# Kernel tuning notes

Measured on AMD Instinct MI355X. Metric: run time of the kernel, lower is better.

The kernel has to match this reference:

```python
import jax, jax.numpy as jnp
import numpy as np
import math

D_MODEL = 2048
N_HEADS = 16
D_K = D_MODEL // N_HEADS
B = 4
S = 2048


def setup_inputs() -> dict:
    key = jax.random.key(0)
    ks = jax.random.split(key, 12)
    sd = 1.0 / math.sqrt(D_MODEL)
    inp = {
        "query": jax.random.normal(ks[0], (B, S, D_MODEL), dtype=jnp.float32),
        "key": jax.random.normal(ks[1], (B, S, D_MODEL), dtype=jnp.float32),
        "value": jax.random.normal(ks[2], (B, S, D_MODEL), dtype=jnp.float32),
        # causal mask: 1 where attendable, 0 where masked (mask == 0 -> -1e9)
        "mask": jnp.tril(jnp.ones((1, 1, S, S), dtype=jnp.int32)),
        "W_q": jax.random.uniform(ks[3], (D_MODEL, D_MODEL), jnp.float32, -sd, sd),
        "b_q": jnp.zeros((D_MODEL,), jnp.float32),
        "W_k": jax.random.uniform(ks[4], (D_MODEL, D_MODEL), jnp.float32, -sd, sd),
        "b_k": jnp.zeros((D_MODEL,), jnp.float32),
        "W_v": jax.random.uniform(ks[5], (D_MODEL, D_MODEL), jnp.float32, -sd, sd),
        "b_v": jnp.zeros((D_MODEL,), jnp.float32),
        "W_o": jax.random.uniform(ks[6], (D_MODEL, D_MODEL), jnp.float32, -sd, sd),
        "b_o": jnp.zeros((D_MODEL,), jnp.float32),
    }
    return inp


def reference(query, key, value, mask, W_q, b_q, W_k, b_k, W_v, b_v, W_o, b_o):
    scale = math.sqrt(D_K)
    # QKV projections + split heads: [B, S, D] -> [B, H, S, d_k]
    def split_heads(x):
        return x.reshape(B, -1, N_HEADS, D_K).transpose(0, 2, 1, 3)

    Q = split_heads(query @ W_q.T + b_q)
    K = split_heads(key @ W_k.T + b_k)
    V = split_heads(value @ W_v.T + b_v)

    # scores: [B, H, Sq, Sk]
    scores = jnp.einsum("bhqd,bhkd->bhqk", Q, K) / scale
    scores = jnp.where(mask == 0, jnp.float32(-1e9), scores)
    attn = jax.nn.softmax(scores, axis=-1)
    # context: [B, H, Sq, d_k] -> [B, Sq, D]
    ctx = jnp.einsum("bhqk,bhkd->bhqd", attn, V)
    ctx = ctx.transpose(0, 2, 1, 3).reshape(B, S, D_MODEL)
    return ctx @ W_o.T + b_o
```

## Files before the change

### kernel.cpp

```cpp
#include <hip/hip_runtime.h>
#include <stdint.h>

#define D_MODEL 2048
#define S_LEN 2048
#define BATCH 4
#define NHEADS 16
#define DK 128
#define M_TOK (BATCH * S_LEN)

typedef __attribute__((ext_vector_type(8))) short bf16x8;
typedef __attribute__((ext_vector_type(4))) float f32x4;

__device__ __forceinline__ short f2bf(float f) {
  unsigned u = __float_as_uint(f);
  u = (u + 0x7FFF + ((u >> 16) & 1)) >> 16;
  return (short)u;
}

__device__ __forceinline__ void gl2lds16(const void* g, void* l) {
  __builtin_amdgcn_global_load_lds(
      (const __attribute__((address_space(1))) unsigned int*)g,
      (__attribute__((address_space(3))) unsigned int*)l, 16, 0, 0);
}

#define ASM_BAR() asm volatile("s_barrier" ::: "memory")
#define VMCNT2() asm volatile("s_waitcnt vmcnt(2)" ::: "memory")
#define VMCNT0() asm volatile("s_waitcnt vmcnt(0)" ::: "memory")

__global__ __launch_bounds__(256) void cvt_kernel(const float* __restrict__ in,
                                                  short* __restrict__ out,
                                                  int n8) {
  int i = blockIdx.x * blockDim.x + threadIdx.x;
  const int stride = gridDim.x * blockDim.x;
  for (; i < n8; i += stride) {
    const float4* p = (const float4*)(in + (size_t)i * 8);
    float4 a = p[0], b = p[1];
    bf16x8 o;
    o[0] = f2bf(a.x); o[1] = f2bf(a.y); o[2] = f2bf(a.z); o[3] = f2bf(a.w);
    o[4] = f2bf(b.x); o[5] = f2bf(b.y); o[6] = f2bf(b.z); o[7] = f2bf(b.w);
    *(bf16x8*)(out + (size_t)i * 8) = o;
  }
}

template <int EPI>
__global__ __launch_bounds__(512, 2) void gemm256(const short* __restrict__ A,
                                                  const short* __restrict__ B,
                                                  const float* __restrict__ bias,
                                                  void* __restrict__ Cout) {
  __shared__ short As[2][256 * 64];
  __shared__ short Bs[2][256 * 64];
  const int t = threadIdx.x, lane = t & 63, w = t >> 6;
  const int c = lane & 15, g = lane >> 4;
  const int wr = w >> 2, wc = w & 3;

  const int cpx = (int)gridDim.x >> 3;
  const int swz = ((int)blockIdx.x & 7) * cpx + ((int)blockIdx.x >> 3);
  const int by = swz >> 3, bx = swz & 7;
  const int row0 = by * 256, col0 = bx * 256;
  const int K = D_MODEL;
  const int NT = K / 64;

  const int srow = t >> 3;
  const int sseg = t & 7;
  const int skk = 8 * (sseg ^ (srow & 7));

  const short* Abase = A + (size_t)(row0 + srow) * K;
  const short* Bbase = B + (size_t)(col0 + srow) * K;

#define SWEEPA(p, R, kt)                                              \
  gl2lds16(Abase + (size_t)(R) * 64 * K + (kt) * 64 + skk,            \
           &As[p][(R) * 4096 + t * 8])
#define SWEEPB(p, R, kt)                                              \
  gl2lds16(Bbase + (size_t)(R) * 64 * K + (kt) * 64 + skk,            \
           &Bs[p][(R) * 4096 + t * 8])

  f32x4 acc[8][4] = {};
  bf16x8 af[4], bf[4];

  auto ldA = [&](int p, int mg, int ks) {
    const char* base = (const char*)As[p];
    const int kb = (ks * 64 + g * 16) ^ ((c & 7) << 4);
#pragma unroll
    for (int mi = 0; mi < 4; ++mi) {
      const int row = wr * 128 + mg * 64 + mi * 16 + c;
      af[mi] = *(const bf16x8*)(base + row * 128 + kb);
    }
  };
  auto ldB = [&](int p, int ks) {
    const char* base = (const char*)Bs[p];
    const int kb = (ks * 64 + g * 16) ^ ((c & 7) << 4);
#pragma unroll
    for (int ni = 0; ni < 4; ++ni) {
      const int row = wc * 64 + ni * 16 + c;
      bf[ni] = *(const bf16x8*)(base + row * 128 + kb);
    }
  };

#define MFMA16(MG)                                                         \
  {                                                                        \
    __builtin_amdgcn_s_setprio(1);                                         \
    _Pragma("unroll") for (int mi = 0; mi < 4; ++mi) {                     \
      _Pragma("unroll") for (int ni = 0; ni < 4; ++ni) {                   \
        acc[(MG) * 4 + mi][ni] = __builtin_amdgcn_mfma_f32_16x16x32_bf16(  \
            af[mi], bf[ni], acc[(MG) * 4 + mi][ni], 0, 0, 0);              \
      }                                                                    \
    }                                                                      \
    __builtin_amdgcn_s_setprio(0);                                         \
    __builtin_amdgcn_sched_barrier(0);                                     \
  }

  SWEEPA(0, 0, 0); SWEEPA(0, 1, 0); SWEEPA(0, 2, 0); SWEEPA(0, 3, 0);
  SWEEPB(0, 0, 0); SWEEPB(0, 1, 0); SWEEPB(0, 2, 0); SWEEPB(0, 3, 0);
  VMCNT0();
  ASM_BAR();

  for (int kt = 0; kt < NT; ++kt) {
    const int p = kt & 1, q = p ^ 1;
    const bool more = (kt + 1 < NT);
    ldA(p, 0, 0); ldB(p, 0);
    if (more) {
      SWEEPA(q, 0, kt + 1); SWEEPA(q, 2, kt + 1);
      VMCNT2();
    } else {
      VMCNT0();
    }
    ASM_BAR();
    MFMA16(0);
    ASM_BAR();
    ldA(p, 1, 0);
    if (more) { SWEEPB(q, 0, kt + 1); SWEEPB(q, 1, kt + 1); }
    ASM_BAR();
    MFMA16(1);
    ASM_BAR();
    ldA(p, 0, 1); ldB(p, 1);
    if (more) { SWEEPB(q, 2, kt + 1); SWEEPB(q, 3, kt + 1); }
    ASM_BAR();
    MFMA16(0);
    ASM_BAR();
    ldA(p, 1, 1);
    if (more) {
      SWEEPA(q, 1, kt + 1); SWEEPA(q, 3, kt + 1);
      VMCNT2();
    }
    ASM_BAR();
    MFMA16(1);
    ASM_BAR();
  }

#pragma unroll
  for (int ni = 0; ni < 4; ++ni) {
    const int col = col0 + wc * 64 + ni * 16 + c;
    const float bv = bias[col];
#pragma unroll
    for (int m = 0; m < 8; ++m) {
      const int rbase = row0 + wr * 128 + (m >> 2) * 64 + (m & 3) * 16 + g * 4;
#pragma unroll
      for (int r = 0; r < 4; ++r) {
        const int row = rbase + r;
        const float v = acc[m][ni][r] + bv;
        if (EPI == 0) {
          const int b = row >> 11, s = row & 2047;
          const int h = col >> 7, dk = col & 127;
          ((short*)Cout)[(((size_t)b * NHEADS + h) * S_LEN + s) * DK + dk] =
              f2bf(v);
        } else {
          ((float*)Cout)[(size_t)row * D_MODEL + col] = v;
        }
      }
    }
  }
#undef SWEEPA
#undef SWEEPB
#undef MFMA16
}

__global__ __launch_bounds__(256) void transpose_v(const short* __restrict__ V,
                                                   short* __restrict__ Vt) {
  __shared__ short tile[64][72];
  const int t = threadIdx.x;
  const int s0 = blockIdx.x * 64, d0 = blockIdx.y * 64;
  const int bh = blockIdx.z;
  const short* Vg = V + (size_t)bh * S_LEN * DK;
  short* Vo = Vt + (size_t)bh * DK * S_LEN;
#pragma unroll
  for (int i = 0; i < 2; ++i) {
    int sg = t + 256 * i;
    int row = sg >> 3, cs = sg & 7;
    *(bf16x8*)&tile[row][cs * 8] =
        *(const bf16x8*)&Vg[(size_t)(s0 + row) * DK + d0 + cs * 8];
  }
  __syncthreads();
#pragma unroll
  for (int i = 0; i < 2; ++i) {
    int sg = t + 256 * i;
    int dr = sg >> 3, cs = sg & 7;
    bf16x8 v;
#pragma unroll
    for (int jj = 0; jj < 8; ++jj) v[jj] = tile[cs * 8 + jj][dr];
    *(bf16x8*)&Vo[(size_t)(d0 + dr) * S_LEN + s0 + cs * 8] = v;
  }
}

__global__ __launch_bounds__(256, 2) void attn_kernel(
    const short* __restrict__ Qp, const short* __restrict__ Kp,
    const short* __restrict__ Vt, short* __restrict__ ctx) {
  const int t = threadIdx.x, lane = t & 63, w = t >> 6;
  const int c = lane & 15, g = lane >> 4;

  const int fid = blockIdx.x;
  const int x = fid & 7, u = fid >> 3;
  const int bh = ((u & 7) << 3) | x;
  const int qt = 15 - (u >> 3);
  const int b = bh >> 4, h = bh & 15;

  __shared__ short Kl[2][64 * 128];
  __shared__ short Vl[2][128 * 64];
  __shared__ short Pl[4][32][64];

  const short* Kbase = Kp + (size_t)bh * S_LEN * DK;
  const short* Vbase = Vt + (size_t)bh * DK * S_LEN;

  const int qbase = qt * 128 + w * 32;
  const short* Qg = Qp + ((size_t)bh * S_LEN + qbase + c) * DK;
  bf16x8 aq[2][4];
#pragma unroll
  for (int mi = 0; mi < 2; ++mi)
#pragma unroll
    for (int kc = 0; kc < 4; ++kc)
      aq[mi][kc] = *(const bf16x8*)(Qg + mi * 16 * DK + kc * 32 + g * 8);

  float mprev[2][4], lsum[2][4];
  f32x4 accO[2][8] = {};
#pragma unroll
  for (int mi = 0; mi < 2; ++mi)
#pragma unroll
    for (int r = 0; r < 4; ++r) {
      mprev[mi][r] = -3.0e38f;
      lsum[mi][r] = 0.f;
    }
  const float cexp = 0.12753101829629947f;

  const int nt = 2 * qt + 2;
  const int jmax = (qbase + 31) >> 6;

  auto stage = [&](int buf, int j) {
    const short* Kg = Kbase + (size_t)j * 64 * DK;
#pragma unroll
    for (int ii = 0; ii < 4; ++ii) {
      int s = t + 256 * ii;
      int row = s >> 4, cs = s & 15;
      gl2lds16(Kg + row * DK + (cs ^ (row & 7)) * 8, &Kl[buf][s * 8]);
    }
    const short* Vg = Vbase + j * 64;
#pragma unroll
    for (int ii = 0; ii < 4; ++ii) {
      int s = t + 256 * ii;
      int row = s >> 3, cs = s & 7;
      gl2lds16(Vg + (size_t)row * S_LEN + (cs ^ (row & 7)) * 8,
               &Vl[buf][s * 8]);
    }
  };

  stage(0, 0);
  __syncthreads();
  int cur = 0;

  for (int j = 0; j < nt; ++j) {
    if (j + 1 < nt) stage(cur ^ 1, j + 1);

    if (j <= jmax) {
      f32x4 sa[2][4];
#pragma unroll
      for (int mi = 0; mi < 2; ++mi)
#pragma unroll
        for (int nf = 0; nf < 4; ++nf) sa[mi][nf] = (f32x4){0.f, 0.f, 0.f, 0.f};
      __builtin_amdgcn_s_setprio(1);
#pragma unroll
      for (int nf = 0; nf < 4; ++nf) {
#pragma unroll
        for (int kc = 0; kc < 4; ++kc) {
          const int row = nf * 16 + c;
          const int seg = kc * 4 + g;
          bf16x8 bk = *(const bf16x8*)((const char*)&Kl[cur][0] + row * 256 +
                                       ((seg ^ (row & 7)) << 4));
#pragma unroll
          for (int mi = 0; mi < 2; ++mi)
            sa[mi][nf] = __builtin_amdgcn_mfma_f32_16x16x32_bf16(
                aq[mi][kc], bk, sa[mi][nf], 0, 0, 0);
        }
      }
      __builtin_amdgcn_s_setprio(0);

#pragma unroll
      for (int mi = 0; mi < 2; ++mi) {
        if (j * 64 + 63 > qbase + mi * 16) {
#pragma unroll
          for (int r = 0; r < 4; ++r) {
            const int qglob = qbase + mi * 16 + g * 4 + r;
#pragma unroll
            for (int nf = 0; nf < 4; ++nf)
              if ((j * 64 + nf * 16 + c) > qglob) sa[mi][nf][r] = -3.0e38f;
          }
        }
      }

      float mt[2][4];
      bool need = false;
#pragma unroll
      for (int mi = 0; mi < 2; ++mi)
#pragma unroll
        for (int r = 0; r < 4; ++r) {
          float m0 = fmaxf(fmaxf(sa[mi][0][r], sa[mi][1][r]),
                           fmaxf(sa[mi][2][r], sa[mi][3][r]));
          m0 = fmaxf(m0, __shfl_xor(m0, 1));
          m0 = fmaxf(m0, __shfl_xor(m0, 2));
          m0 = fmaxf(m0, __shfl_xor(m0, 4));
          m0 = fmaxf(m0, __shfl_xor(m0, 8));
          mt[mi][r] = m0;
          need = need || (m0 > mprev[mi][r] + 40.f);
        }
      const bool full = __any((int)need);

#pragma unroll
      for (int mi = 0; mi < 2; ++mi)
#pragma unroll
        for (int r = 0; r < 4; ++r) {
          float nm = mprev[mi][r];
          if (full) {
            nm = fmaxf(nm, mt[mi][r]);
            const float corr = exp2f((mprev[mi][r] - nm) * cexp);
            lsum[mi][r] *= corr;
#pragma unroll
            for (int no = 0; no < 8; ++no) accO[mi][no][r] *= corr;
            mprev[mi][r] = nm;
          }
          const int prow = mi * 16 + g * 4 + r;
          float rs = 0.f;
#pragma unroll
          for (int nf = 0; nf < 4; ++nf) {
            const float pp = exp2f((sa[mi][nf][r] - nm) * cexp);
            rs += pp;
            const int col = nf * 16 + c;
            *(short*)((char*)&Pl[w][0][0] + prow * 128 +
                      (((col >> 3) ^ (prow & 7)) << 4) + (col & 7) * 2) =
                f2bf(pp);
          }
          rs += __shfl_xor(rs, 1);
          rs += __shfl_xor(rs, 2);
          rs += __shfl_xor(rs, 4);
          rs += __shfl_xor(rs, 8);
          lsum[mi][r] += rs;
        }

      bf16x8 ap[2][2];
#pragma unroll
      for (int mi = 0; mi < 2; ++mi)
#pragma unroll
        for (int kc = 0; kc < 2; ++kc) {
          const int prow = mi * 16 + c;
          const int kseg = kc * 4 + g;
          ap[mi][kc] = *(const bf16x8*)((const char*)&Pl[w][0][0] +
                                        prow * 128 +
                                        ((kseg ^ (prow & 7)) << 4));
        }
      __builtin_amdgcn_s_setprio(1);
#pragma unroll
      for (int no = 0; no < 8; ++no) {
#pragma unroll
        for (int kc = 0; kc < 2; ++kc) {
          const int row = no * 16 + c;
          const int seg = kc * 4 + g;
          bf16x8 bv = *(const bf16x8*)((const char*)&Vl[cur][0] + row * 128 +
                                       ((seg ^ (row & 7)) << 4));
#pragma unroll
          for (int mi = 0; mi < 2; ++mi)
            accO[mi][no] = __builtin_amdgcn_mfma_f32_16x16x32_bf16(
                ap[mi][kc], bv, accO[mi][no], 0, 0, 0);
        }
      }
      __builtin_amdgcn_s_setprio(0);
    }

    __syncthreads();
    cur ^= 1;
  }

#pragma unroll
  for (int mi = 0; mi < 2; ++mi) {
    const int qrow = qbase + mi * 16 + g * 4;
#pragma unroll
    for (int r = 0; r < 4; ++r) {
      const float inv = 1.f / lsum[mi][r];
#pragma unroll
      for (int no = 0; no < 8; ++no) {
        ctx[((size_t)b * S_LEN + qrow + r) * D_MODEL + h * DK + no * 16 + c] =
            f2bf(accO[mi][no][r] * inv);
      }
    }
  }
}

extern "C" void kernel_launch(void* const* d_in, const int* in_sizes, int n_in,
                              void* d_out, int out_size, void* d_ws,
                              size_t ws_size, hipStream_t stream) {
  const float* query = (const float*)d_in[0];
  const float* key = (const float*)d_in[1];
  const float* value = (const float*)d_in[2];
  const float* W_q = (const float*)d_in[4];
  const float* b_q = (const float*)d_in[5];
  const float* W_k = (const float*)d_in[6];
  const float* b_k = (const float*)d_in[7];
  const float* W_v = (const float*)d_in[8];
  const float* b_v = (const float*)d_in[9];
  const float* W_o = (const float*)d_in[10];
  const float* b_o = (const float*)d_in[11];
  float* out = (float*)d_out;

  char* p = (char*)d_ws;
  const size_t WSZ = (size_t)D_MODEL * D_MODEL * 2;
  const size_t XSZ = (size_t)M_TOK * D_MODEL * 2;
  short* wq = (short*)p; p += WSZ;
  short* wk = (short*)p; p += WSZ;
  short* wv = (short*)p; p += WSZ;
  short* wo = (short*)p; p += WSZ;
  short* xq = (short*)p; p += XSZ;
  short* xk = (short*)p; p += XSZ;
  short* xv = (short*)p; p += XSZ;
  short* Qp = (short*)p; p += XSZ;
  short* Kp = (short*)p; p += XSZ;
  short* Vp = (short*)p; p += XSZ;

  const int nX8 = (M_TOK * D_MODEL) / 8;
  const int nW8 = (D_MODEL * D_MODEL) / 8;
  cvt_kernel<<<2048, 256, 0, stream>>>(query, xq, nX8);
  cvt_kernel<<<2048, 256, 0, stream>>>(key, xk, nX8);
  cvt_kernel<<<2048, 256, 0, stream>>>(value, xv, nX8);
  cvt_kernel<<<2048, 256, 0, stream>>>(W_q, wq, nW8);
  cvt_kernel<<<2048, 256, 0, stream>>>(W_k, wk, nW8);
  cvt_kernel<<<2048, 256, 0, stream>>>(W_v, wv, nW8);
  cvt_kernel<<<2048, 256, 0, stream>>>(W_o, wo, nW8);

  const int ngemm = (M_TOK / 256) * (D_MODEL / 256);
  gemm256<0><<<ngemm, 512, 0, stream>>>(xq, wq, b_q, Qp);
  gemm256<0><<<ngemm, 512, 0, stream>>>(xk, wk, b_k, Kp);
  gemm256<0><<<ngemm, 512, 0, stream>>>(xv, wv, b_v, Vp);

  transpose_v<<<dim3(S_LEN / 64, DK / 64, BATCH * NHEADS), 256, 0, stream>>>(Vp, xk);

  attn_kernel<<<dim3(16 * BATCH * NHEADS), 256, 0, stream>>>(Qp, Kp, xk, xq);

  gemm256<1><<<ngemm, 512, 0, stream>>>(xq, wo, b_o, out);
}
```

Measured before the change: 556.8 us.

## Fuse V transpose into projection GEMM epilogue and simplify GEMM pipeline

Adds an EPI==2 GEMM epilogue that writes the V projection directly in transposed [b,h,dk,s] layout as packed 4-element bf16 stores. This removes the separate transpose_v kernel and the intermediate Vp buffer round-trip. The GEMM main loop is also restructured: instead of interleaving partial next-tile loads between four MFMA phases with partial vmcnt waits, each iteration now waits for all loads, issues the whole next tile at once, then computes both k-halves. That coarser double buffering may expose more load latency per iteration in exchange for fewer barriers and simpler scheduling.

```diff
diff --git a/kernel.cpp b/kernel.cpp
--- a/kernel.cpp
+++ b/kernel.cpp
@@ -24,7 +24,6 @@
 }
 
 #define ASM_BAR() asm volatile("s_barrier" ::: "memory")
-#define VMCNT2() asm volatile("s_waitcnt vmcnt(2)" ::: "memory")
 #define VMCNT0() asm volatile("s_waitcnt vmcnt(0)" ::: "memory")
 
 __global__ __launch_bounds__(256) void cvt_kernel(const float* __restrict__ in,
@@ -73,78 +72,51 @@
 #define SWEEPB(p, R, kt)                                              \
   gl2lds16(Bbase + (size_t)(R) * 64 * K + (kt) * 64 + skk,            \
            &Bs[p][(R) * 4096 + t * 8])
+#define STAGE_TILE(q, kt1)                                            \
+  {                                                                   \
+    SWEEPA(q, 0, kt1); SWEEPA(q, 1, kt1);                             \
+    SWEEPA(q, 2, kt1); SWEEPA(q, 3, kt1);                             \
+    SWEEPB(q, 0, kt1); SWEEPB(q, 1, kt1);                             \
+    SWEEPB(q, 2, kt1); SWEEPB(q, 3, kt1);                             \
+  }
 
   f32x4 acc[8][4] = {};
-  bf16x8 af[4], bf[4];
-
-  auto ldA = [&](int p, int mg, int ks) {
-    const char* base = (const char*)As[p];
-    const int kb = (ks * 64 + g * 16) ^ ((c & 7) << 4);
-#pragma unroll
-    for (int mi = 0; mi < 4; ++mi) {
-      const int row = wr * 128 + mg * 64 + mi * 16 + c;
-      af[mi] = *(const bf16x8*)(base + row * 128 + kb);
-    }
-  };
-  auto ldB = [&](int p, int ks) {
-    const char* base = (const char*)Bs[p];
-    const int kb = (ks * 64 + g * 16) ^ ((c & 7) << 4);
-#pragma unroll
-    for (int ni = 0; ni < 4; ++ni) {
-      const int row = wc * 64 + ni * 16 + c;
-      bf[ni] = *(const bf16x8*)(base + row * 128 + kb);
-    }
-  };
-
-#define MFMA16(MG)                                                         \
-  {                                                                        \
-    __builtin_amdgcn_s_setprio(1);                                         \
-    _Pragma("unroll") for (int mi = 0; mi < 4; ++mi) {                     \
-      _Pragma("unroll") for (int ni = 0; ni < 4; ++ni) {                   \
-        acc[(MG) * 4 + mi][ni] = __builtin_amdgcn_mfma_f32_16x16x32_bf16(  \
-            af[mi], bf[ni], acc[(MG) * 4 + mi][ni], 0, 0, 0);              \
-      }                                                                    \
-    }                                                                      \
-    __builtin_amdgcn_s_setprio(0);                                         \
-    __builtin_amdgcn_sched_barrier(0);                                     \
-  }
-
-  SWEEPA(0, 0, 0); SWEEPA(0, 1, 0); SWEEPA(0, 2, 0); SWEEPA(0, 3, 0);
-  SWEEPB(0, 0, 0); SWEEPB(0, 1, 0); SWEEPB(0, 2, 0); SWEEPB(0, 3, 0);
-  VMCNT0();
-  ASM_BAR();
+
+  STAGE_TILE(0, 0);
 
   for (int kt = 0; kt < NT; ++kt) {
     const int p = kt & 1, q = p ^ 1;
-    const bool more = (kt + 1 < NT);
-    ldA(p, 0, 0); ldB(p, 0);
-    if (more) {
-      SWEEPA(q, 0, kt + 1); SWEEPA(q, 2, kt + 1);
-      VMCNT2();
-    } else {
-      VMCNT0();
-    }
+    VMCNT0();
     ASM_BAR();
-    MFMA16(0);
-    ASM_BAR();
-    ldA(p, 1, 0);
-    if (more) { SWEEPB(q, 0, kt + 1); SWEEPB(q, 1, kt + 1); }
-    ASM_BAR();
-    MFMA16(1);
-    ASM_BAR();
-    ldA(p, 0, 1); ldB(p, 1);
-    if (more) { SWEEPB(q, 2, kt + 1); SWEEPB(q, 3, kt + 1); }
-    ASM_BAR();
-    MFMA16(0);
-    ASM_BAR();
-    ldA(p, 1, 1);
-    if (more) {
-      SWEEPA(q, 1, kt + 1); SWEEPA(q, 3, kt + 1);
-      VMCNT2();
-    }
-    ASM_BAR();
-    MFMA16(1);
-    ASM_BAR();
+    if (kt + 1 < NT) STAGE_TILE(q, kt + 1);
+
+    const char* abase = (const char*)As[p];
+    const char* bbase = (const char*)Bs[p];
+#pragma unroll
+    for (int ks = 0; ks < 2; ++ks) {
+      const int kb = (ks * 64 + g * 16) ^ ((c & 7) << 4);
+      bf16x8 bfr[4];
+#pragma unroll
+      for (int ni = 0; ni < 4; ++ni)
+        bfr[ni] = *(const bf16x8*)(bbase + (wc * 64 + ni * 16 + c) * 128 + kb);
+#pragma unroll
+      for (int mg = 0; mg < 2; ++mg) {
+        bf16x8 afr[4];
+#pragma unroll
+        for (int mi = 0; mi < 4; ++mi)
+          afr[mi] = *(const bf16x8*)(abase +
+                                     (wr * 128 + mg * 64 + mi * 16 + c) * 128 +
+                                     kb);
+        __builtin_amdgcn_s_setprio(1);
+#pragma unroll
+        for (int mi = 0; mi < 4; ++mi)
+#pragma unroll
+          for (int ni = 0; ni < 4; ++ni)
+            acc[mg * 4 + mi][ni] = __builtin_amdgcn_mfma_f32_16x16x32_bf16(
+                afr[mi], bfr[ni], acc[mg * 4 + mi][ni], 0, 0, 0);
+        __builtin_amdgcn_s_setprio(0);
+      }
+    }
   }
 
 #pragma unroll
@@ -154,51 +126,36 @@
 #pragma unroll
     for (int m = 0; m < 8; ++m) {
       const int rbase = row0 + wr * 128 + (m >> 2) * 64 + (m & 3) * 16 + g * 4;
-#pragma unroll
-      for (int r = 0; r < 4; ++r) {
-        const int row = rbase + r;
-        const float v = acc[m][ni][r] + bv;
-        if (EPI == 0) {
-          const int b = row >> 11, s = row & 2047;
-          const int h = col >> 7, dk = col & 127;
-          ((short*)Cout)[(((size_t)b * NHEADS + h) * S_LEN + s) * DK + dk] =
-              f2bf(v);
-        } else {
-          ((float*)Cout)[(size_t)row * D_MODEL + col] = v;
+      if (EPI == 2) {
+        const int h = col >> 7, dk = col & 127;
+        const int b = rbase >> 11, s0 = rbase & 2047;
+        ushort4 pk;
+        pk.x = (unsigned short)f2bf(acc[m][ni][0] + bv);
+        pk.y = (unsigned short)f2bf(acc[m][ni][1] + bv);
+        pk.z = (unsigned short)f2bf(acc[m][ni][2] + bv);
+        pk.w = (unsigned short)f2bf(acc[m][ni][3] + bv);
+        *(ushort4*)&((short*)Cout)[(((size_t)b * NHEADS + h) * DK + dk) *
+                                       S_LEN + s0] = pk;
+      } else {
+#pragma unroll
+        for (int r = 0; r < 4; ++r) {
+          const int row = rbase + r;
+          const float v = acc[m][ni][r] + bv;
+          if (EPI == 0) {
+            const int b = row >> 11, s = row & 2047;
+            const int h = col >> 7, dk = col & 127;
+            ((short*)Cout)[(((size_t)b * NHEADS + h) * S_LEN + s) * DK + dk] =
+                f2bf(v);
+          } else {
+            ((float*)Cout)[(size_t)row * D_MODEL + col] = v;
+          }
         }
       }
     }
   }
 #undef SWEEPA
 #undef SWEEPB
-#undef MFMA16
-}
-
-__global__ __launch_bounds__(256) void transpose_v(const short* __restrict__ V,
-                                                   short* __restrict__ Vt) {
-  __shared__ short tile[64][72];
-  const int t = threadIdx.x;
-  const int s0 = blockIdx.x * 64, d0 = blockIdx.y * 64;
-  const int bh = blockIdx.z;
-  const short* Vg = V + (size_t)bh * S_LEN * DK;
-  short* Vo = Vt + (size_t)bh * DK * S_LEN;
-#pragma unroll
-  for (int i = 0; i < 2; ++i) {
-    int sg = t + 256 * i;
-    int row = sg >> 3, cs = sg & 7;
-    *(bf16x8*)&tile[row][cs * 8] =
-        *(const bf16x8*)&Vg[(size_t)(s0 + row) * DK + d0 + cs * 8];
-  }
-  __syncthreads();
-#pragma unroll
-  for (int i = 0; i < 2; ++i) {
-    int sg = t + 256 * i;
-    int dr = sg >> 3, cs = sg & 7;
-    bf16x8 v;
-#pragma unroll
-    for (int jj = 0; jj < 8; ++jj) v[jj] = tile[cs * 8 + jj][dr];
-    *(bf16x8*)&Vo[(size_t)(d0 + dr) * S_LEN + s0 + cs * 8] = v;
-  }
+#undef STAGE_TILE
 }
 
 __global__ __launch_bounds__(256, 2) void attn_kernel(
@@ -428,7 +385,6 @@
   short* xv = (short*)p; p += XSZ;
   short* Qp = (short*)p; p += XSZ;
   short* Kp = (short*)p; p += XSZ;
-  short* Vp = (short*)p; p += XSZ;
 
   const int nX8 = (M_TOK * D_MODEL) / 8;
   const int nW8 = (D_MODEL * D_MODEL) / 8;
@@ -443,9 +399,7 @@
   const int ngemm = (M_TOK / 256) * (D_MODEL / 256);
   gemm256<0><<<ngemm, 512, 0, stream>>>(xq, wq, b_q, Qp);
   gemm256<0><<<ngemm, 512, 0, stream>>>(xk, wk, b_k, Kp);
-  gemm256<0><<<ngemm, 512, 0, stream>>>(xv, wv, b_v, Vp);
-
-  transpose_v<<<dim3(S_LEN / 64, DK / 64, BATCH * NHEADS), 256, 0, stream>>>(Vp, xk);
+  gemm256<2><<<ngemm, 512, 0, stream>>>(xv, wv, b_v, xk);
 
   attn_kernel<<<dim3(16 * BATCH * NHEADS), 256, 0, stream>>>(Qp, Kp, xk, xq);
 
```

Measured after the change: 533.5 us. 4.2% less time.
